# Kernel optimization log

Measured on AMD Instinct MI355X. Metric: run time of the kernel, lower is better.

The kernel has to match this reference:

```python
import jax, jax.numpy as jnp
import numpy as np

B = 4          # per_gpu_batch_size
P = 16         # n_contexts
N = B * P      # fused passage dim = 64
L = 512        # seq_len
H = 768        # hidden_size
S = 16         # sentence spans per passage


def setup_inputs() -> dict:
    key = jax.random.key(0)
    k1, k2, k3 = jax.random.split(key, 3)
    hidden_states = jax.random.normal(k1, (N, L, H), jnp.float32)
    # nn.Linear weight [out, in]; original init std=1.0 saturates tanh, use 0.02 scale for sane numerics
    dense_w = jax.random.normal(k2, (H, H), jnp.float32) * 0.02
    dense_b = jnp.zeros((H,), jnp.float32)
    attention_mask = jnp.ones((N, L), jnp.int32)
    # strictly increasing boundaries -> S non-empty, ragged, contiguous spans per passage
    r = jnp.sort(jax.random.randint(k3, (N, S + 1), 0, L - S), axis=-1) + jnp.arange(S + 1, dtype=jnp.int32)
    spans = jnp.stack([r[:, :-1], r[:, 1:]], axis=-1).astype(jnp.int32)  # [N, S, 2]
    return dict(hidden_states=hidden_states, dense_w=dense_w, dense_b=dense_b,
                attention_mask=attention_mask, spans=spans)


def reference(hidden_states, dense_w, dense_b, attention_mask, spans):
    # sentence_spans branch: token_tensor = hidden_states (all tokens)
    # pooled_output = activation(dense(token_tensor)); cls_norm_type == 'none' -> no norm
    pooled = jnp.tanh(jnp.einsum('nlh,oh->nlo', hidden_states, dense_w) + dense_b)  # [N, L, H]
    pooled_output_passages = pooled[:, 0]  # [N, H]
    # ragged per-span mean pooling, vectorized as a masked segment reduce
    pos = jnp.arange(L, dtype=jnp.int32)                         # [L]
    start = spans[..., 0][..., None]                             # [N, S, 1]
    end = spans[..., 1][..., None]                               # [N, S, 1]
    m = ((pos >= start) & (pos < end)).astype(pooled.dtype)      # [N, S, L]
    sums = jnp.einsum('nsl,nlh->nsh', m, pooled)                 # [N, S, H]
    counts = (spans[..., 1] - spans[..., 0]).astype(pooled.dtype)[..., None]  # [N, S, 1]
    sentence_embeddings = (sums / counts).reshape(N * S, H)      # [N*S, H]
    # all S spans valid per passage -> mask of zeros (0 = valid in original code)
    sentence_mask = jnp.zeros((N, S), jnp.float32)
    return pooled_output_passages, sentence_embeddings, sentence_mask
```

## Files before the change

kernel.cpp:

```cpp
#include <hip/hip_runtime.h>
#include <hip/hip_bf16.h>

#define NPASS 64
#define LSEQ  512
#define HDIM  768
#define NSPAN 16
#define MTOT  (NPASS*LSEQ)
#define OFF_SENT (NPASS*HDIM)
#define OFF_MASK (OFF_SENT + NPASS*NSPAN*HDIM)
#define A_ELEMS (MTOT*HDIM)
#define W_ELEMS (HDIM*HDIM)

#define BN   96
#define NTN  6
#define BK   32
#define NK   (HDIM/BK)
#define NTILES (HDIM/BN)
#define NBLK 256
#define THREADS 512
#define NMT  4

typedef __bf16 bf16x8 __attribute__((ext_vector_type(8)));
typedef __bf16 bf16x4 __attribute__((ext_vector_type(4)));
typedef float  f32x4  __attribute__((ext_vector_type(4)));

__device__ inline unsigned short f2bf(float f) {
  __hip_bfloat16 h = __float2bfloat16(f);
  unsigned short u; __builtin_memcpy(&u, &h, 2); return u;
}

__device__ inline float fast_tanh(float x) {
  const float ax = fabsf(x);
  const float t  = __expf(-2.0f * ax);
  const float r  = (1.0f - t) * __builtin_amdgcn_rcpf(1.0f + t);
  return copysignf(r, x);
}

__global__ __launch_bounds__(256) void convert_kernel(
    const float* __restrict__ A, const float* __restrict__ W,
    unsigned short* __restrict__ Ab, unsigned short* __restrict__ Wb)
{
  const long long i = ((long long)blockIdx.x * 256 + threadIdx.x) * 8;
  const float* src; unsigned short* dst; long long off;
  if (i < A_ELEMS) { src = A; dst = Ab; off = i; }
  else             { src = W; dst = Wb; off = i - A_ELEMS; }
  const float4 a = *(const float4*)(src + off);
  const float4 b = *(const float4*)(src + off + 4);
  union { unsigned short us[8]; uint4 v; } o;
  o.us[0]=f2bf(a.x); o.us[1]=f2bf(a.y); o.us[2]=f2bf(a.z); o.us[3]=f2bf(a.w);
  o.us[4]=f2bf(b.x); o.us[5]=f2bf(b.y); o.us[6]=f2bf(b.z); o.us[7]=f2bf(b.w);
  *(uint4*)(dst + off) = o.v;
}

__global__ __launch_bounds__(THREADS, 2) void fused_kernel(
    const unsigned short* __restrict__ Ab,
    const unsigned short* __restrict__ Wb,
    const float* __restrict__ bias,
    const int*   __restrict__ spans,
    float* __restrict__ out)
{
  __shared__ __align__(16) unsigned short Wl[BN * HDIM];
  __shared__ float sent_lds[NSPAN][BN];
  __shared__ float inv_s[NSPAN];
  __shared__ float bias_s[BN];
  __shared__ short sid_l[LSEQ];

  const int tid = threadIdx.x;
  const int b   = blockIdx.x;
  const int xcd = b & 7;
  const int t   = b >> 3;
  const int p0  = ((t >> 3) << 3) | xcd;
  const int ntb = t & 7;
  const int tile_n = ntb * BN;

  const int wave = tid >> 6;
  const int lane = tid & 63;
  const int quad = lane >> 4;
  const int lr   = lane & 15;

  {
    #pragma unroll
    for (int j = 0; j < (BN * (HDIM / 8)) / THREADS; ++j) {
      const int gi = j * THREADS + tid;
      const int wr = gi / (HDIM / 8);
      const int kg = gi % (HDIM / 8);
      const unsigned short* src =
          Wb + (size_t)(tile_n + wr) * HDIM + ((kg ^ (wr & 7)) * 8);
      __builtin_amdgcn_global_load_lds(
          (const __attribute__((address_space(1))) void*)src,
          (__attribute__((address_space(3))) void*)(Wl + (size_t)gi * 8),
          16, 0, 0);
    }
  }
  if (tid < BN) bias_s[tid] = bias[tile_n + tid];

  for (int pi = 0; pi < 2; ++pi) {
    const int p = p0 + pi * 32;

    {
      int st[NSPAN], en[NSPAN];
      #pragma unroll
      for (int i = 0; i < NSPAN; ++i) {
        st[i] = spans[(p * NSPAN + i) * 2 + 0];
        en[i] = spans[(p * NSPAN + i) * 2 + 1];
      }
      short s = -1;
      #pragma unroll
      for (int i = 0; i < NSPAN; ++i)
        if (tid >= st[i] && tid < en[i]) s = (short)i;
      sid_l[tid] = s;
    }
    if (tid < NSPAN)
      inv_s[tid] = 1.0f / (float)(spans[(p * NSPAN + tid) * 2 + 1] -
                                  spans[(p * NSPAN + tid) * 2 + 0]);
    for (int i = tid; i < NSPAN * BN; i += THREADS) (&sent_lds[0][0])[i] = 0.f;

    __syncthreads();

    const unsigned short* Abp =
        Ab + ((size_t)p * LSEQ + wave * 64 + lr) * HDIM + quad * 8;

    f32x4 acc[NMT][NTN];
    #pragma unroll
    for (int mt = 0; mt < NMT; ++mt)
      #pragma unroll
      for (int nt = 0; nt < NTN; ++nt)
        acc[mt][nt] = (f32x4){0.f, 0.f, 0.f, 0.f};

    bf16x8 a_cur[NMT], a_nxt[NMT];
    #pragma unroll
    for (int mt = 0; mt < NMT; ++mt)
      a_cur[mt] = *(const bf16x8*)(Abp + (size_t)mt * 16 * HDIM);

    #pragma unroll
    for (int k = 0; k < NK; ++k) {
      bf16x8 wf[NTN];
      #pragma unroll
      for (int nt = 0; nt < NTN; ++nt) {
        const int wr = nt * 16 + lr;
        const int kg = (4 * k + quad) ^ (lr & 7);
        wf[nt] = *(const bf16x8*)(Wl + (size_t)wr * HDIM + kg * 8);
      }
      if (k + 1 < NK) {
        #pragma unroll
        for (int mt = 0; mt < NMT; ++mt)
          a_nxt[mt] = *(const bf16x8*)(Abp + (size_t)mt * 16 * HDIM + (k + 1) * BK);
      }
      __builtin_amdgcn_s_setprio(1);
      #pragma unroll
      for (int mt = 0; mt < NMT; ++mt)
        #pragma unroll
        for (int nt = 0; nt < NTN; ++nt)
          acc[mt][nt] = __builtin_amdgcn_mfma_f32_16x16x32_bf16(
              a_cur[mt], wf[nt], acc[mt][nt], 0, 0, 0);
      __builtin_amdgcn_s_setprio(0);
      #pragma unroll
      for (int mt = 0; mt < NMT; ++mt) a_cur[mt] = a_nxt[mt];
    }

    #pragma unroll
    for (int nt = 0; nt < NTN; ++nt) {
      const int col = nt * 16 + lr;
      const float bv = bias_s[col];
      #pragma unroll
      for (int mt = 0; mt < NMT; ++mt) {
        const int rowbase = wave * 64 + mt * 16 + quad * 4;
        int prev = -1; float run = 0.f;
        #pragma unroll
        for (int r = 0; r < 4; ++r) {
          const int row = rowbase + r;
          const float v = fast_tanh(acc[mt][nt][r] + bv);
          if (row == 0) out[(size_t)p * HDIM + tile_n + col] = v;
          const int s = sid_l[row];
          if (s != prev) {
            if (prev >= 0) atomicAdd(&sent_lds[prev][col], run);
            prev = s; run = 0.f;
          }
          run += v;
        }
        if (prev >= 0) atomicAdd(&sent_lds[prev][col], run);
      }
    }
    __syncthreads();

    for (int i = tid; i < NSPAN * BN; i += THREADS) {
      const int s = i / BN, c = i % BN;
      out[OFF_SENT + ((size_t)p * NSPAN + s) * HDIM + tile_n + c] =
          sent_lds[s][c] * inv_s[s];
    }
    if (ntb == 0 && tid < NSPAN) out[OFF_MASK + p * NSPAN + tid] = 0.f;

    __syncthreads();
  }
}

extern "C" void kernel_launch(void* const* d_in, const int* in_sizes, int n_in,
                              void* d_out, int out_size, void* d_ws, size_t ws_size,
                              hipStream_t stream) {
  const float* hs  = (const float*)d_in[0];
  const float* w   = (const float*)d_in[1];
  const float* bsc = (const float*)d_in[2];
  const int* spans = (const int*)d_in[4];

  unsigned short* Ab = (unsigned short*)d_ws;
  unsigned short* Wb = Ab + A_ELEMS;

  convert_kernel<<<dim3((A_ELEMS + W_ELEMS) / 8 / 256), dim3(256), 0, stream>>>(
      hs, w, Ab, Wb);

  fused_kernel<<<dim3(NBLK), dim3(THREADS), 0, stream>>>(
      Ab, Wb, bsc, spans, (float*)d_out);
}
```

Before: 231.0 us.

## Split passages into half-sequence chunks with global atomic span accumulation

Each block now processes four 256-row half-passages instead of two full passages, halving per-wave M tiles (NMT 4→2) to cut accumulator register pressure. Span sums are accumulated directly into global memory with unsafeAtomicAdd pre-scaled by the inverse span length, removing the LDS reduction buffer and its extra barrier and writeback pass. The A operand prefetch is deepened to two stages. Output is zeroed with a memset beforehand, which adds a full-output clear and global atomic traffic. The explicit zero write of the sentence mask now relies on that memset.

```diff
diff --git a/kernel.cpp b/kernel.cpp
--- a/kernel.cpp
+++ b/kernel.cpp
@@ -7,7 +7,6 @@
 #define NSPAN 16
 #define MTOT  (NPASS*LSEQ)
 #define OFF_SENT (NPASS*HDIM)
-#define OFF_MASK (OFF_SENT + NPASS*NSPAN*HDIM)
 #define A_ELEMS (MTOT*HDIM)
 #define W_ELEMS (HDIM*HDIM)
 
@@ -15,10 +14,10 @@
 #define NTN  6
 #define BK   32
 #define NK   (HDIM/BK)
-#define NTILES (HDIM/BN)
 #define NBLK 256
 #define THREADS 512
-#define NMT  4
+#define NMT  2
+#define CROWS 256
 
 typedef __bf16 bf16x8 __attribute__((ext_vector_type(8)));
 typedef __bf16 bf16x4 __attribute__((ext_vector_type(4)));
@@ -60,17 +59,16 @@
     float* __restrict__ out)
 {
   __shared__ __align__(16) unsigned short Wl[BN * HDIM];
-  __shared__ float sent_lds[NSPAN][BN];
   __shared__ float inv_s[NSPAN];
   __shared__ float bias_s[BN];
-  __shared__ short sid_l[LSEQ];
-
-  const int tid = threadIdx.x;
-  const int b   = blockIdx.x;
-  const int xcd = b & 7;
-  const int t   = b >> 3;
-  const int p0  = ((t >> 3) << 3) | xcd;
-  const int ntb = t & 7;
+  __shared__ short sid_l[CROWS];
+
+  const int tid  = threadIdx.x;
+  const int b    = blockIdx.x;
+  const int xcd  = b & 7;
+  const int t    = b >> 3;
+  const int ntb  = t & 7;
+  const int slot = t >> 3;
   const int tile_n = ntb * BN;
 
   const int wave = tid >> 6;
@@ -94,31 +92,29 @@
   }
   if (tid < BN) bias_s[tid] = bias[tile_n + tid];
 
-  for (int pi = 0; pi < 2; ++pi) {
-    const int p = p0 + pi * 32;
-
-    {
-      int st[NSPAN], en[NSPAN];
+  for (int pi = 0; pi < 4; ++pi) {
+    const int h  = pi * 4 + slot;
+    const int p  = xcd + 8 * (h >> 1);
+    const int l0 = (h & 1) * CROWS;
+
+    if (tid < CROWS) {
+      const int l = l0 + tid;
+      short s = -1;
       #pragma unroll
       for (int i = 0; i < NSPAN; ++i) {
-        st[i] = spans[(p * NSPAN + i) * 2 + 0];
-        en[i] = spans[(p * NSPAN + i) * 2 + 1];
-      }
-      short s = -1;
-      #pragma unroll
-      for (int i = 0; i < NSPAN; ++i)
-        if (tid >= st[i] && tid < en[i]) s = (short)i;
+        const int st = spans[(p * NSPAN + i) * 2 + 0];
+        const int en = spans[(p * NSPAN + i) * 2 + 1];
+        if (l >= st && l < en) s = (short)i;
+      }
       sid_l[tid] = s;
     }
     if (tid < NSPAN)
       inv_s[tid] = 1.0f / (float)(spans[(p * NSPAN + tid) * 2 + 1] -
                                   spans[(p * NSPAN + tid) * 2 + 0]);
-    for (int i = tid; i < NSPAN * BN; i += THREADS) (&sent_lds[0][0])[i] = 0.f;
-
     __syncthreads();
 
     const unsigned short* Abp =
-        Ab + ((size_t)p * LSEQ + wave * 64 + lr) * HDIM + quad * 8;
+        Ab + ((size_t)p * LSEQ + l0 + wave * 32 + lr) * HDIM + quad * 8;
 
     f32x4 acc[NMT][NTN];
     #pragma unroll
@@ -127,13 +123,16 @@
       for (int nt = 0; nt < NTN; ++nt)
         acc[mt][nt] = (f32x4){0.f, 0.f, 0.f, 0.f};
 
-    bf16x8 a_cur[NMT], a_nxt[NMT];
-    #pragma unroll
-    for (int mt = 0; mt < NMT; ++mt)
-      a_cur[mt] = *(const bf16x8*)(Abp + (size_t)mt * 16 * HDIM);
+    bf16x8 areg[2][NMT];
+    #pragma unroll
+    for (int mt = 0; mt < NMT; ++mt) {
+      areg[0][mt] = *(const bf16x8*)(Abp + (size_t)mt * 16 * HDIM);
+      areg[1][mt] = *(const bf16x8*)(Abp + (size_t)mt * 16 * HDIM + BK);
+    }
 
     #pragma unroll
     for (int k = 0; k < NK; ++k) {
+      const int q = k & 1;
       bf16x8 wf[NTN];
       #pragma unroll
       for (int nt = 0; nt < NTN; ++nt) {
@@ -141,10 +140,13 @@
         const int kg = (4 * k + quad) ^ (lr & 7);
         wf[nt] = *(const bf16x8*)(Wl + (size_t)wr * HDIM + kg * 8);
       }
-      if (k + 1 < NK) {
+      bf16x8 a_use[NMT];
+      #pragma unroll
+      for (int mt = 0; mt < NMT; ++mt) a_use[mt] = areg[q][mt];
+      if (k + 2 < NK) {
         #pragma unroll
         for (int mt = 0; mt < NMT; ++mt)
-          a_nxt[mt] = *(const bf16x8*)(Abp + (size_t)mt * 16 * HDIM + (k + 1) * BK);
+          areg[q][mt] = *(const bf16x8*)(Abp + (size_t)mt * 16 * HDIM + (k + 2) * BK);
       }
       __builtin_amdgcn_s_setprio(1);
       #pragma unroll
@@ -152,44 +154,34 @@
         #pragma unroll
         for (int nt = 0; nt < NTN; ++nt)
           acc[mt][nt] = __builtin_amdgcn_mfma_f32_16x16x32_bf16(
-              a_cur[mt], wf[nt], acc[mt][nt], 0, 0, 0);
+              a_use[mt], wf[nt], acc[mt][nt], 0, 0, 0);
       __builtin_amdgcn_s_setprio(0);
-      #pragma unroll
-      for (int mt = 0; mt < NMT; ++mt) a_cur[mt] = a_nxt[mt];
     }
 
     #pragma unroll
     for (int nt = 0; nt < NTN; ++nt) {
-      const int col = nt * 16 + lr;
-      const float bv = bias_s[col];
+      const int col = tile_n + nt * 16 + lr;
+      const float bv = bias_s[nt * 16 + lr];
+      float* sent_col = out + OFF_SENT + (size_t)(p * NSPAN) * HDIM + col;
       #pragma unroll
       for (int mt = 0; mt < NMT; ++mt) {
-        const int rowbase = wave * 64 + mt * 16 + quad * 4;
+        const int rowbase = wave * 32 + mt * 16 + quad * 4;
         int prev = -1; float run = 0.f;
         #pragma unroll
         for (int r = 0; r < 4; ++r) {
           const int row = rowbase + r;
           const float v = fast_tanh(acc[mt][nt][r] + bv);
-          if (row == 0) out[(size_t)p * HDIM + tile_n + col] = v;
+          if (l0 == 0 && row == 0) out[(size_t)p * HDIM + col] = v;
           const int s = sid_l[row];
           if (s != prev) {
-            if (prev >= 0) atomicAdd(&sent_lds[prev][col], run);
+            if (prev >= 0) unsafeAtomicAdd(sent_col + (size_t)prev * HDIM, run * inv_s[prev]);
             prev = s; run = 0.f;
           }
           run += v;
         }
-        if (prev >= 0) atomicAdd(&sent_lds[prev][col], run);
-      }
-    }
-    __syncthreads();
-
-    for (int i = tid; i < NSPAN * BN; i += THREADS) {
-      const int s = i / BN, c = i % BN;
-      out[OFF_SENT + ((size_t)p * NSPAN + s) * HDIM + tile_n + c] =
-          sent_lds[s][c] * inv_s[s];
-    }
-    if (ntb == 0 && tid < NSPAN) out[OFF_MASK + p * NSPAN + tid] = 0.f;
-
+        if (prev >= 0) unsafeAtomicAdd(sent_col + (size_t)prev * HDIM, run * inv_s[prev]);
+      }
+    }
     __syncthreads();
   }
 }
@@ -201,13 +193,16 @@
   const float* w   = (const float*)d_in[1];
   const float* bsc = (const float*)d_in[2];
   const int* spans = (const int*)d_in[4];
+  float* out = (float*)d_out;
 
   unsigned short* Ab = (unsigned short*)d_ws;
   unsigned short* Wb = Ab + A_ELEMS;
 
+  hipMemsetAsync(d_out, 0, (size_t)out_size * sizeof(float), stream);
+
   convert_kernel<<<dim3((A_ELEMS + W_ELEMS) / 8 / 256), dim3(256), 0, stream>>>(
       hs, w, Ab, Wb);
 
   fused_kernel<<<dim3(NBLK), dim3(THREADS), 0, stream>>>(
-      Ab, Wb, bsc, spans, (float*)d_out);
-}
+      Ab, Wb, bsc, spans, out);
+}
```

After: 268.2 us. +16.1%, slower.
